# Kernel optimization log

Measured on AMD Instinct MI355X. Metric: run time of the kernel, lower is better.

## Reference

```python
import jax, jax.numpy as jnp
import numpy as np

SEQ_LEN = 28
EMBED = 28
HIDDEN = 256
OUT = 10
BATCH = 32768


def _orthogonal(key, rows, cols):
    # mimic torch orthogonal init via QR
    a = jax.random.normal(key, (max(rows, cols), min(rows, cols)), dtype=jnp.float32)
    q, r = jnp.linalg.qr(a)
    q = q * jnp.sign(jnp.diagonal(r))
    if rows < cols:
        q = q.T
    return q[:rows, :cols]


def setup_inputs() -> dict:
    key = jax.random.key(0)
    ks = jax.random.split(key, 7)
    seq = jax.random.normal(ks[0], (BATCH, SEQ_LEN, EMBED), dtype=jnp.float32)
    bound1 = 1.0 / np.sqrt(EMBED)
    bound2 = 1.0 / np.sqrt(HIDDEN)
    return {
        "seq": seq,
        "W1": _orthogonal(ks[1], HIDDEN, EMBED),            # linear1.weight [H, E]
        "b1": jax.random.uniform(ks[2], (HIDDEN,), minval=-bound1, maxval=bound1),
        "W2": _orthogonal(ks[3], HIDDEN, HIDDEN),           # linear2.weight [H, H]
        "b2": jax.random.uniform(ks[4], (HIDDEN,), minval=-bound2, maxval=bound2),
        "W3": _orthogonal(ks[5], OUT, HIDDEN),              # linear3.weight [O, H]
        "b3": jax.random.uniform(ks[6], (OUT,), minval=-bound2, maxval=bound2),
    }


def reference(seq, W1, b1, W2, b2, W3, b3):
    B = seq.shape[0]
    seq = seq.reshape(B, SEQ_LEN, -1)
    # precompute input projection for all steps: [B, T, H]
    x_proj = jnp.einsum("bte,he->bth", seq, W1) + b1
    h0 = jnp.zeros((B, HIDDEN), dtype=seq.dtype)

    def step(h, xp_t):
        h = jnp.tanh(xp_t + h @ W2.T + b2)
        return h, None

    h, _ = jax.lax.scan(step, h0, jnp.swapaxes(x_proj, 0, 1))  # scan over T
    return h @ W3.T + b3
```

## Files before the change

### kernel.cpp

```cpp
#include <hip/hip_runtime.h>
#include <hip/hip_bf16.h>

#define T_LEN 28
#define EMB   28
#define HID   256
#define NOUT  10
#define BATCH 32768
#define SCALE 2.8853900817779268f

typedef _Float16 f16x8  __attribute__((ext_vector_type(8)));
typedef _Float16 f16x4  __attribute__((ext_vector_type(4)));
typedef float    f32x4  __attribute__((ext_vector_type(4)));
typedef float    f32x16 __attribute__((ext_vector_type(16)));

__global__ __launch_bounds__(256) void prep_kernel(
    const float* __restrict__ W1, const float* __restrict__ W2,
    const float* __restrict__ b1, const float* __restrict__ b2,
    _Float16* __restrict__ W2A, _Float16* __restrict__ W1A) {
    int idx = blockIdx.x * 256 + threadIdx.x;
    if (idx < 65536) {
        int q  = idx & 7;
        int lm = (idx >> 3) & 63;
        int kb = (idx >> 9) & 15;
        int jt = idx >> 13;
        int j  = jt * 32 + (lm & 31);
        int k  = kb * 16 + (lm >> 5) * 8 + q;
        W2A[idx] = (_Float16)(SCALE * W2[j * HID + k]);
    }
    if (idx < 8192) {
        int q  = idx & 7;
        int lm = (idx >> 3) & 63;
        int kb = (idx >> 9) & 1;
        int jt = idx >> 10;
        int j  = jt * 32 + (lm & 31);
        int e  = kb * 16 + (lm >> 5) * 8 + q;
        float v = (e < EMB) ? SCALE * W1[j * EMB + e]
                            : (e == EMB ? SCALE * (b1[j] + b2[j]) : 0.f);
        W1A[idx] = (_Float16)v;
    }
}

__global__ __launch_bounds__(256, 2) void rnn_kernel(
    const float* __restrict__ seq,
    const _Float16* __restrict__ W2A,
    const _Float16* __restrict__ W1A,
    const float* __restrict__ W3,
    const float* __restrict__ b3,
    float* __restrict__ out)
{
    __shared__ __align__(16) char hls[2][16384];

    const int tid = threadIdx.x;
    const int l   = tid & 63;
    const int wv  = tid >> 6;
    const int lo  = l & 31;
    const int hi  = l >> 5;
    const int r0  = blockIdx.x * 32;

    f16x8 w2f[2][16];
#pragma unroll
    for (int a = 0; a < 2; ++a)
#pragma unroll
        for (int kb = 0; kb < 16; ++kb)
            w2f[a][kb] = *(const f16x8*)(W2A + ((((wv * 2 + a) * 16 + kb) * 64 + l) * 8));
    f16x8 w1f[2][2];
#pragma unroll
    for (int a = 0; a < 2; ++a)
#pragma unroll
        for (int kb = 0; kb < 2; ++kb)
            w1f[a][kb] = *(const f16x8*)(W1A + ((((wv * 2 + a) * 2 + kb) * 64 + l) * 8));

    int wOff[2][4];
#pragma unroll
    for (int a = 0; a < 2; ++a)
#pragma unroll
        for (int q = 0; q < 4; ++q)
            wOff[a][q] = (((wv * 2 + a) * 4 + q) * 32 + lo) * 16 + hi * 8;

    const float* rowp = seq + (size_t)(r0 + lo) * (T_LEN * EMB);

    auto tanh4 = [&](float v0, float v1, float v2, float v3) -> f16x4 {
        f16x4 hv;
        float vv[4] = {v0, v1, v2, v3};
#pragma unroll
        for (int r = 0; r < 4; ++r) {
            float e  = __builtin_amdgcn_exp2f(vv[r]);
            float rc = __builtin_amdgcn_rcpf(e + 1.f);
            vv[r] = __builtin_fmaf(-2.f, rc, 1.f);
        }
#pragma unroll
        for (int r = 0; r < 4; ++r) hv[r] = (_Float16)vv[r];
        return hv;
    };

    const f32x16 z = (f32x16)(0.f);

    for (int t = 0; t < T_LEN; ++t) {
        const float* sp  = rowp + t * EMB + hi * 8;
        const float* sp2 = rowp + t * EMB + 16 + hi * 8;
        f32x4 rA = *(const f32x4*)sp;
        f32x4 rB = *(const f32x4*)(sp + 4);
        f32x4 rC = *(const f32x4*)sp2;
        f32x4 rD = (f32x4){1.f, 0.f, 0.f, 0.f};
        if (hi == 0) rD = *(const f32x4*)(sp2 + 4);

        f32x16 acc[2];
        if (t > 0) {
            const char* rp = hls[(t + 1) & 1] + l * 16;
            __builtin_amdgcn_s_setprio(1);
#pragma unroll
            for (int kb = 0; kb < 16; ++kb) {
                f16x8 hB = *(const f16x8*)(rp + kb * 1024);
#pragma unroll
                for (int a = 0; a < 2; ++a)
                    acc[a] = __builtin_amdgcn_mfma_f32_32x32x16_f16(
                                 w2f[a][kb], hB, (kb == 0) ? z : acc[a], 0, 0, 0);
            }
            __builtin_amdgcn_s_setprio(0);
        }

        f16x8 xf0, xf1;
#pragma unroll
        for (int q2 = 0; q2 < 4; ++q2) {
            xf0[q2] = (_Float16)rA[q2]; xf0[4 + q2] = (_Float16)rB[q2];
            xf1[q2] = (_Float16)rC[q2]; xf1[4 + q2] = (_Float16)rD[q2];
        }
#pragma unroll
        for (int a = 0; a < 2; ++a) {
            acc[a] = __builtin_amdgcn_mfma_f32_32x32x16_f16(w1f[a][0], xf0,
                         (t == 0) ? z : acc[a], 0, 0, 0);
            acc[a] = __builtin_amdgcn_mfma_f32_32x32x16_f16(w1f[a][1], xf1, acc[a], 0, 0, 0);
        }

        char* wb = hls[t & 1];
#pragma unroll
        for (int a = 0; a < 2; ++a)
#pragma unroll
            for (int q = 0; q < 4; ++q)
                *(f16x4*)(wb + wOff[a][q]) =
                    tanh4(acc[a][q * 4 + 0], acc[a][q * 4 + 1],
                          acc[a][q * 4 + 2], acc[a][q * 4 + 3]);
        __syncthreads();
    }

    const char* hb = hls[(T_LEN - 1) & 1];
    for (int idx = tid; idx < 32 * NOUT; idx += 256) {
        int i = idx / NOUT;
        int o = idx - i * NOUT;
        float s = b3[o];
#pragma unroll
        for (int c = 0; c < 32; ++c) {
            f16x8 hv  = *(const f16x8*)(hb + c * 512 + i * 16);
            f32x4 w0  = *(const f32x4*)(W3 + o * HID + c * 8);
            f32x4 w1v = *(const f32x4*)(W3 + o * HID + c * 8 + 4);
#pragma unroll
            for (int q = 0; q < 4; ++q)
                s += (float)hv[q] * w0[q] + (float)hv[4 + q] * w1v[q];
        }
        out[(size_t)(r0 + i) * NOUT + o] = s;
    }
}

extern "C" void kernel_launch(void* const* d_in, const int* in_sizes, int n_in,
                              void* d_out, int out_size, void* d_ws, size_t ws_size,
                              hipStream_t stream) {
    const float* seq = (const float*)d_in[0];
    const float* W1  = (const float*)d_in[1];
    const float* b1  = (const float*)d_in[2];
    const float* W2  = (const float*)d_in[3];
    const float* b2  = (const float*)d_in[4];
    const float* W3  = (const float*)d_in[5];
    const float* b3  = (const float*)d_in[6];
    float* outp = (float*)d_out;

    _Float16* W2A = (_Float16*)d_ws;
    _Float16* W1A = (_Float16*)((char*)d_ws + 65536 * sizeof(_Float16));

    prep_kernel<<<256, 256, 0, stream>>>(W1, W2, b1, b2, W2A, W1A);
    rnn_kernel<<<BATCH / 32, 256, 0, stream>>>(seq, W2A, W1A, W3, b3, outp);
}
```

Measured before the change: 171.5 us.

## Interleave two batch tiles per block to overlap tanh with MFMA

Each block now handles 64 rows as two independent 32-row groups using 512 threads (8 waves), each wave owning one 32-column hidden tile. The two groups are ping-ponged, so the tanh and LDS store of one group overlaps the recurrent MFMA chain of the other, and input loads are prefetched a step ahead. The aim is to hide the serial tanh/store latency between timesteps and halve the W2 registers per wave. The cost is more waves per block, which may limit occupancy under the stated launch bounds, and the same number of barriers per step.

```diff
diff --git a/kernel.cpp b/kernel.cpp
--- a/kernel.cpp
+++ b/kernel.cpp
@@ -40,7 +40,7 @@
     }
 }
 
-__global__ __launch_bounds__(256, 2) void rnn_kernel(
+__global__ __launch_bounds__(512, 2) void rnn_kernel(
     const float* __restrict__ seq,
     const _Float16* __restrict__ W2A,
     const _Float16* __restrict__ W1A,
@@ -55,102 +55,119 @@
     const int wv  = tid >> 6;
     const int lo  = l & 31;
     const int hi  = l >> 5;
-    const int r0  = blockIdx.x * 32;
+    const int r0  = blockIdx.x * 64;
 
-    f16x8 w2f[2][16];
+    f16x8 w2f[16];
 #pragma unroll
-    for (int a = 0; a < 2; ++a)
+    for (int kb = 0; kb < 16; ++kb)
+        w2f[kb] = *(const f16x8*)(W2A + (((wv * 16 + kb) * 64 + l) * 8));
+    f16x8 w1f[2];
 #pragma unroll
-        for (int kb = 0; kb < 16; ++kb)
-            w2f[a][kb] = *(const f16x8*)(W2A + ((((wv * 2 + a) * 16 + kb) * 64 + l) * 8));
-    f16x8 w1f[2][2];
+    for (int kb = 0; kb < 2; ++kb)
+        w1f[kb] = *(const f16x8*)(W1A + (((wv * 2 + kb) * 64 + l) * 8));
+
+    const int wbase = (wv * 128 + lo) * 16 + hi * 8;
+
+    const float* rowA = seq + (size_t)(r0 + lo) * (T_LEN * EMB);
+    const float* rowB = seq + (size_t)(r0 + 32 + lo) * (T_LEN * EMB);
+
+    auto load_raw = [&](const float* rowp, int t, f32x4 r[4]) {
+        const float* sp  = rowp + t * EMB + hi * 8;
+        const float* sp2 = rowp + t * EMB + 16 + hi * 8;
+        r[0] = *(const f32x4*)sp;
+        r[1] = *(const f32x4*)(sp + 4);
+        r[2] = *(const f32x4*)sp2;
+        if (hi == 0) r[3] = *(const f32x4*)(sp2 + 4);
+        else         r[3] = (f32x4){1.f, 0.f, 0.f, 0.f};
+    };
+    auto cvt_x = [&](const f32x4 r[4], f16x8& x0, f16x8& x1) {
 #pragma unroll
-    for (int a = 0; a < 2; ++a)
+        for (int q = 0; q < 4; ++q) {
+            x0[q] = (_Float16)r[0][q]; x0[4 + q] = (_Float16)r[1][q];
+            x1[q] = (_Float16)r[2][q]; x1[4 + q] = (_Float16)r[3][q];
+        }
+    };
+    auto tanh_store = [&](const f32x16& acc, char* buf) {
 #pragma unroll
-        for (int kb = 0; kb < 2; ++kb)
-            w1f[a][kb] = *(const f16x8*)(W1A + ((((wv * 2 + a) * 2 + kb) * 64 + l) * 8));
-
-    int wOff[2][4];
+        for (int q = 0; q < 4; ++q) {
+            f16x4 hv;
 #pragma unroll
-    for (int a = 0; a < 2; ++a)
-#pragma unroll
-        for (int q = 0; q < 4; ++q)
-            wOff[a][q] = (((wv * 2 + a) * 4 + q) * 32 + lo) * 16 + hi * 8;
-
-    const float* rowp = seq + (size_t)(r0 + lo) * (T_LEN * EMB);
-
-    auto tanh4 = [&](float v0, float v1, float v2, float v3) -> f16x4 {
-        f16x4 hv;
-        float vv[4] = {v0, v1, v2, v3};
-#pragma unroll
-        for (int r = 0; r < 4; ++r) {
-            float e  = __builtin_amdgcn_exp2f(vv[r]);
-            float rc = __builtin_amdgcn_rcpf(e + 1.f);
-            vv[r] = __builtin_fmaf(-2.f, rc, 1.f);
+            for (int r = 0; r < 4; ++r) {
+                float e  = __builtin_amdgcn_exp2f(acc[q * 4 + r]);
+                float rc = __builtin_amdgcn_rcpf(e + 1.f);
+                hv[r] = (_Float16)__builtin_fmaf(-2.f, rc, 1.f);
+            }
+            *(f16x4*)(buf + wbase + q * 512) = hv;
         }
-#pragma unroll
-        for (int r = 0; r < 4; ++r) hv[r] = (_Float16)vv[r];
-        return hv;
     };
 
     const f32x16 z = (f32x16)(0.f);
+    f32x16 accA, accB;
+    f32x4 ra[4], rb[4];
 
-    for (int t = 0; t < T_LEN; ++t) {
-        const float* sp  = rowp + t * EMB + hi * 8;
-        const float* sp2 = rowp + t * EMB + 16 + hi * 8;
-        f32x4 rA = *(const f32x4*)sp;
-        f32x4 rB = *(const f32x4*)(sp + 4);
-        f32x4 rC = *(const f32x4*)sp2;
-        f32x4 rD = (f32x4){1.f, 0.f, 0.f, 0.f};
-        if (hi == 0) rD = *(const f32x4*)(sp2 + 4);
+    {
+        load_raw(rowA, 0, ra);
+        load_raw(rowB, 0, rb);
+        f16x8 xa0, xa1, xb0, xb1;
+        cvt_x(ra, xa0, xa1);
+        cvt_x(rb, xb0, xb1);
+        load_raw(rowA, 1, ra);
+        accA = __builtin_amdgcn_mfma_f32_32x32x16_f16(w1f[0], xa0, z, 0, 0, 0);
+        accA = __builtin_amdgcn_mfma_f32_32x32x16_f16(w1f[1], xa1, accA, 0, 0, 0);
+        accB = __builtin_amdgcn_mfma_f32_32x32x16_f16(w1f[0], xb0, z, 0, 0, 0);
+        accB = __builtin_amdgcn_mfma_f32_32x32x16_f16(w1f[1], xb1, accB, 0, 0, 0);
+        tanh_store(accA, hls[0]);
+    }
+    __syncthreads();
 
-        f32x16 acc[2];
-        if (t > 0) {
-            const char* rp = hls[(t + 1) & 1] + l * 16;
-            __builtin_amdgcn_s_setprio(1);
+    for (int t = 1; t < T_LEN; ++t) {
+        {
+            f16x8 xa0, xa1;
+            cvt_x(ra, xa0, xa1);
+            load_raw(rowB, t, rb);
+            const char* rp = hls[0] + l * 16;
 #pragma unroll
             for (int kb = 0; kb < 16; ++kb) {
                 f16x8 hB = *(const f16x8*)(rp + kb * 1024);
+                accA = __builtin_amdgcn_mfma_f32_32x32x16_f16(
+                           w2f[kb], hB, (kb == 0) ? z : accA, 0, 0, 0);
+            }
+            tanh_store(accB, hls[1]);
+            accA = __builtin_amdgcn_mfma_f32_32x32x16_f16(w1f[0], xa0, accA, 0, 0, 0);
+            accA = __builtin_amdgcn_mfma_f32_32x32x16_f16(w1f[1], xa1, accA, 0, 0, 0);
+        }
+        __syncthreads();
+
+        {
+            f16x8 xb0, xb1;
+            cvt_x(rb, xb0, xb1);
+            load_raw(rowA, (t < T_LEN - 1) ? t + 1 : t, ra);
+            const char* rp = hls[1] + l * 16;
 #pragma unroll
-                for (int a = 0; a < 2; ++a)
-                    acc[a] = __builtin_amdgcn_mfma_f32_32x32x16_f16(
-                                 w2f[a][kb], hB, (kb == 0) ? z : acc[a], 0, 0, 0);
+            for (int kb = 0; kb < 16; ++kb) {
+                f16x8 hB = *(const f16x8*)(rp + kb * 1024);
+                accB = __builtin_amdgcn_mfma_f32_32x32x16_f16(
+                           w2f[kb], hB, (kb == 0) ? z : accB, 0, 0, 0);
             }
-            __builtin_amdgcn_s_setprio(0);
+            tanh_store(accA, hls[0]);
+            accB = __builtin_amdgcn_mfma_f32_32x32x16_f16(w1f[0], xb0, accB, 0, 0, 0);
+            accB = __builtin_amdgcn_mfma_f32_32x32x16_f16(w1f[1], xb1, accB, 0, 0, 0);
         }
-
-        f16x8 xf0, xf1;
-#pragma unroll
-        for (int q2 = 0; q2 < 4; ++q2) {
-            xf0[q2] = (_Float16)rA[q2]; xf0[4 + q2] = (_Float16)rB[q2];
-            xf1[q2] = (_Float16)rC[q2]; xf1[4 + q2] = (_Float16)rD[q2];
-        }
-#pragma unroll
-        for (int a = 0; a < 2; ++a) {
-            acc[a] = __builtin_amdgcn_mfma_f32_32x32x16_f16(w1f[a][0], xf0,
-                         (t == 0) ? z : acc[a], 0, 0, 0);
-            acc[a] = __builtin_amdgcn_mfma_f32_32x32x16_f16(w1f[a][1], xf1, acc[a], 0, 0, 0);
-        }
-
-        char* wb = hls[t & 1];
-#pragma unroll
-        for (int a = 0; a < 2; ++a)
-#pragma unroll
-            for (int q = 0; q < 4; ++q)
-                *(f16x4*)(wb + wOff[a][q]) =
-                    tanh4(acc[a][q * 4 + 0], acc[a][q * 4 + 1],
-                          acc[a][q * 4 + 2], acc[a][q * 4 + 3]);
         __syncthreads();
     }
 
-    const char* hb = hls[(T_LEN - 1) & 1];
-    for (int idx = tid; idx < 32 * NOUT; idx += 256) {
+    tanh_store(accB, hls[1]);
+    __syncthreads();
+
+    for (int idx = tid; idx < 64 * NOUT; idx += 512) {
         int i = idx / NOUT;
         int o = idx - i * NOUT;
+        const char* hb = hls[i >> 5];
+        int row = i & 31;
         float s = b3[o];
 #pragma unroll
         for (int c = 0; c < 32; ++c) {
-            f16x8 hv  = *(const f16x8*)(hb + c * 512 + i * 16);
+            f16x8 hv  = *(const f16x8*)(hb + c * 512 + row * 16);
             f32x4 w0  = *(const f32x4*)(W3 + o * HID + c * 8);
             f32x4 w1v = *(const f32x4*)(W3 + o * HID + c * 8 + 4);
 #pragma unroll
@@ -177,5 +194,5 @@
     _Float16* W1A = (_Float16*)((char*)d_ws + 65536 * sizeof(_Float16));
 
     prep_kernel<<<256, 256, 0, stream>>>(W1, W2, b1, b2, W2A, W1A);
-    rnn_kernel<<<BATCH / 32, 256, 0, stream>>>(seq, W2A, W1A, W3, b3, outp);
+    rnn_kernel<<<BATCH / 64, 512, 0, stream>>>(seq, W2A, W1A, W3, b3, outp);
 }
```

New measurement: 201.6 us. 17.5% more time.

## Stage W2 in LDS and process 64 rows per 512-thread block

Applied to the files above, without the earlier changes.

Moves the recurrent weight matrix from per-wave registers into a 128KB LDS buffer shared by eight waves, each wave owning 32 hidden units and computing two 32-row batch tiles. Blocks now handle 64 batch rows with 512 threads, and the hidden state uses a single LDS buffer guarded by two barriers per step instead of double buffering. This frees registers and reuses each W2 fragment across two batch tiles, but adds an LDS weight read per MFMA pair, an extra barrier per step, and 160KB of LDS per block, which limits occupancy to one block per CU.

```diff
diff --git a/kernel.cpp b/kernel.cpp
--- a/kernel.cpp
+++ b/kernel.cpp
@@ -40,7 +40,7 @@
     }
 }
 
-__global__ __launch_bounds__(256, 2) void rnn_kernel(
+__global__ __launch_bounds__(512, 2) void rnn_kernel(
     const float* __restrict__ seq,
     const _Float16* __restrict__ W2A,
     const _Float16* __restrict__ W1A,
@@ -48,36 +48,36 @@
     const float* __restrict__ b3,
     float* __restrict__ out)
 {
-    __shared__ __align__(16) char hls[2][16384];
+    __shared__ __align__(16) char lds_[163840];
+    char* const w2l = lds_;
+    char* const hl  = lds_ + 131072;
 
     const int tid = threadIdx.x;
     const int l   = tid & 63;
     const int wv  = tid >> 6;
     const int lo  = l & 31;
     const int hi  = l >> 5;
-    const int r0  = blockIdx.x * 32;
+    const int r0  = blockIdx.x * 64;
 
-    f16x8 w2f[2][16];
+    {
+        const int4* src = (const int4*)W2A;
+        int4*       dst = (int4*)w2l;
 #pragma unroll
-    for (int a = 0; a < 2; ++a)
+        for (int i = 0; i < 16; ++i)
+            dst[tid + i * 512] = src[tid + i * 512];
+    }
+
+    f16x8 w1f[2];
 #pragma unroll
-        for (int kb = 0; kb < 16; ++kb)
-            w2f[a][kb] = *(const f16x8*)(W2A + ((((wv * 2 + a) * 16 + kb) * 64 + l) * 8));
-    f16x8 w1f[2][2];
-#pragma unroll
-    for (int a = 0; a < 2; ++a)
-#pragma unroll
-        for (int kb = 0; kb < 2; ++kb)
-            w1f[a][kb] = *(const f16x8*)(W1A + ((((wv * 2 + a) * 2 + kb) * 64 + l) * 8));
+    for (int kb = 0; kb < 2; ++kb)
+        w1f[kb] = *(const f16x8*)(W1A + (((wv * 2 + kb) * 64 + l) * 8));
 
-    int wOff[2][4];
-#pragma unroll
-    for (int a = 0; a < 2; ++a)
-#pragma unroll
-        for (int q = 0; q < 4; ++q)
-            wOff[a][q] = (((wv * 2 + a) * 4 + q) * 32 + lo) * 16 + hi * 8;
+    const float* rowp0 = seq + (size_t)(r0 + lo) * (T_LEN * EMB);
+    const float* rowp1 = seq + (size_t)(r0 + 32 + lo) * (T_LEN * EMB);
 
-    const float* rowp = seq + (size_t)(r0 + lo) * (T_LEN * EMB);
+    const char* wbase = w2l + wv * 16384 + l * 16;
+    const char* hbase = hl + hi * 1024 + lo * 16;
+    const int wOffBase = ((wv * 4) * 64 + lo) * 16 + hi * 8;
 
     auto tanh4 = [&](float v0, float v1, float v2, float v3) -> f16x4 {
         f16x4 hv;
@@ -95,62 +95,71 @@
 
     const f32x16 z = (f32x16)(0.f);
 
+    __syncthreads();
+
     for (int t = 0; t < T_LEN; ++t) {
-        const float* sp  = rowp + t * EMB + hi * 8;
-        const float* sp2 = rowp + t * EMB + 16 + hi * 8;
-        f32x4 rA = *(const f32x4*)sp;
-        f32x4 rB = *(const f32x4*)(sp + 4);
-        f32x4 rC = *(const f32x4*)sp2;
-        f32x4 rD = (f32x4){1.f, 0.f, 0.f, 0.f};
-        if (hi == 0) rD = *(const f32x4*)(sp2 + 4);
+        const float* s0 = rowp0 + t * EMB;
+        const float* s1 = rowp1 + t * EMB;
+        f32x4 a0 = *(const f32x4*)(s0 + hi * 8);
+        f32x4 a1 = *(const f32x4*)(s0 + hi * 8 + 4);
+        f32x4 a2 = *(const f32x4*)(s0 + 16 + hi * 8);
+        f32x4 a3 = (f32x4){1.f, 0.f, 0.f, 0.f};
+        if (hi == 0) a3 = *(const f32x4*)(s0 + 20);
+        f32x4 b0 = *(const f32x4*)(s1 + hi * 8);
+        f32x4 b1v = *(const f32x4*)(s1 + hi * 8 + 4);
+        f32x4 b2v = *(const f32x4*)(s1 + 16 + hi * 8);
+        f32x4 b3v = (f32x4){1.f, 0.f, 0.f, 0.f};
+        if (hi == 0) b3v = *(const f32x4*)(s1 + 20);
 
-        f32x16 acc[2];
+        f32x16 acc0, acc1;
         if (t > 0) {
-            const char* rp = hls[(t + 1) & 1] + l * 16;
-            __builtin_amdgcn_s_setprio(1);
 #pragma unroll
             for (int kb = 0; kb < 16; ++kb) {
-                f16x8 hB = *(const f16x8*)(rp + kb * 1024);
-#pragma unroll
-                for (int a = 0; a < 2; ++a)
-                    acc[a] = __builtin_amdgcn_mfma_f32_32x32x16_f16(
-                                 w2f[a][kb], hB, (kb == 0) ? z : acc[a], 0, 0, 0);
+                f16x8 wa = *(const f16x8*)(wbase + kb * 1024);
+                f16x8 h0 = *(const f16x8*)(hbase + kb * 2048);
+                f16x8 h1 = *(const f16x8*)(hbase + kb * 2048 + 512);
+                acc0 = __builtin_amdgcn_mfma_f32_32x32x16_f16(wa, h0, (kb == 0) ? z : acc0, 0, 0, 0);
+                acc1 = __builtin_amdgcn_mfma_f32_32x32x16_f16(wa, h1, (kb == 0) ? z : acc1, 0, 0, 0);
             }
-            __builtin_amdgcn_s_setprio(0);
         }
 
-        f16x8 xf0, xf1;
+        f16x8 x00, x01, x10, x11;
 #pragma unroll
-        for (int q2 = 0; q2 < 4; ++q2) {
-            xf0[q2] = (_Float16)rA[q2]; xf0[4 + q2] = (_Float16)rB[q2];
-            xf1[q2] = (_Float16)rC[q2]; xf1[4 + q2] = (_Float16)rD[q2];
+        for (int q = 0; q < 4; ++q) {
+            x00[q] = (_Float16)a0[q]; x00[4 + q] = (_Float16)a1[q];
+            x01[q] = (_Float16)a2[q]; x01[4 + q] = (_Float16)a3[q];
+            x10[q] = (_Float16)b0[q]; x10[4 + q] = (_Float16)b1v[q];
+            x11[q] = (_Float16)b2v[q]; x11[4 + q] = (_Float16)b3v[q];
         }
+        acc0 = __builtin_amdgcn_mfma_f32_32x32x16_f16(w1f[0], x00, (t == 0) ? z : acc0, 0, 0, 0);
+        acc0 = __builtin_amdgcn_mfma_f32_32x32x16_f16(w1f[1], x01, acc0, 0, 0, 0);
+        acc1 = __builtin_amdgcn_mfma_f32_32x32x16_f16(w1f[0], x10, (t == 0) ? z : acc1, 0, 0, 0);
+        acc1 = __builtin_amdgcn_mfma_f32_32x32x16_f16(w1f[1], x11, acc1, 0, 0, 0);
+
+        f16x4 hq0[4], hq1[4];
 #pragma unroll
-        for (int a = 0; a < 2; ++a) {
-            acc[a] = __builtin_amdgcn_mfma_f32_32x32x16_f16(w1f[a][0], xf0,
-                         (t == 0) ? z : acc[a], 0, 0, 0);
-            acc[a] = __builtin_amdgcn_mfma_f32_32x32x16_f16(w1f[a][1], xf1, acc[a], 0, 0, 0);
+        for (int q = 0; q < 4; ++q) {
+            hq0[q] = tanh4(acc0[q * 4], acc0[q * 4 + 1], acc0[q * 4 + 2], acc0[q * 4 + 3]);
+            hq1[q] = tanh4(acc1[q * 4], acc1[q * 4 + 1], acc1[q * 4 + 2], acc1[q * 4 + 3]);
         }
 
-        char* wb = hls[t & 1];
+        __syncthreads();
+
 #pragma unroll
-        for (int a = 0; a < 2; ++a)
-#pragma unroll
-            for (int q = 0; q < 4; ++q)
-                *(f16x4*)(wb + wOff[a][q]) =
-                    tanh4(acc[a][q * 4 + 0], acc[a][q * 4 + 1],
-                          acc[a][q * 4 + 2], acc[a][q * 4 + 3]);
+        for (int q = 0; q < 4; ++q) {
+            *(f16x4*)(hl + wOffBase + q * 1024)       = hq0[q];
+            *(f16x4*)(hl + wOffBase + q * 1024 + 512) = hq1[q];
+        }
         __syncthreads();
     }
 
-    const char* hb = hls[(T_LEN - 1) & 1];
-    for (int idx = tid; idx < 32 * NOUT; idx += 256) {
+    for (int idx = tid; idx < 64 * NOUT; idx += 512) {
         int i = idx / NOUT;
         int o = idx - i * NOUT;
         float s = b3[o];
 #pragma unroll
         for (int c = 0; c < 32; ++c) {
-            f16x8 hv  = *(const f16x8*)(hb + c * 512 + i * 16);
+            f16x8 hv  = *(const f16x8*)(hl + (c * 64 + i) * 16);
             f32x4 w0  = *(const f32x4*)(W3 + o * HID + c * 8);
             f32x4 w1v = *(const f32x4*)(W3 + o * HID + c * 8 + 4);
 #pragma unroll
@@ -177,5 +186,5 @@
     _Float16* W1A = (_Float16*)((char*)d_ws + 65536 * sizeof(_Float16));
 
     prep_kernel<<<256, 256, 0, stream>>>(W1, W2, b1, b2, W2A, W1A);
-    rnn_kernel<<<BATCH / 32, 256, 0, stream>>>(seq, W2A, W1A, W3, b3, outp);
+    rnn_kernel<<<BATCH / 64, 512, 0, stream>>>(seq, W2A, W1A, W3, b3, outp);
 }
```

Measured after the change: 206.9 us. 1.21x slower.
